# Kernel optimization log

Measured on AMD Instinct MI355X. Metric: run time of the kernel, lower is better.

The kernel has to match this reference:

```python
import jax, jax.numpy as jnp
import numpy as np

N, E, C, H, L, G, K, NC = 50000, 500000, 256, 128, 4, 64, 8, 2
EPS_MSG = 1e-7  # GENConv message eps
EPS_BN = 1e-5   # BatchNorm eps


def setup_inputs() -> dict:
    key = jax.random.key(0)
    ks = jax.random.split(key, 32)
    def nrm(k, shape, scale):
        return jax.random.normal(k, shape, dtype=jnp.float32) * scale
    sC = 1.0 / np.sqrt(C).astype(np.float32)
    sH = 1.0 / np.sqrt(H).astype(np.float32)
    s2H = 1.0 / np.sqrt(2 * H).astype(np.float32)
    return dict(
        x=nrm(ks[0], (N, C), 1.0),
        edge_index=jax.random.randint(ks[1], (2, E), 0, N, dtype=jnp.int32),
        edge_attr=jax.random.uniform(ks[2], (E, 1), dtype=jnp.float32),
        batch=jnp.sort(jax.random.randint(ks[3], (N,), 0, G, dtype=jnp.int32)),
        clinical=nrm(ks[4], (G, K), 1.0),
        lin_src_w=nrm(ks[5], (C, H), sC), lin_src_b=nrm(ks[6], (H,), 0.01),
        lin_dst_w=nrm(ks[7], (C, H), sC), lin_dst_b=nrm(ks[8], (H,), 0.01),
        edge_w=nrm(ks[9], (L, 1, H), 1.0), edge_b=nrm(ks[10], (L, H), 0.01),
        t=0.1 + 0.01 * jax.random.normal(ks[11], (L,), dtype=jnp.float32),
        mlp_w1=nrm(ks[12], (L, H, 2 * H), sH), mlp_b1=nrm(ks[13], (L, 2 * H), 0.01),
        mlp_bn_g=1.0 + nrm(ks[14], (L, 2 * H), 0.1), mlp_bn_b=nrm(ks[15], (L, 2 * H), 0.1),
        mlp_bn_m=nrm(ks[16], (L, 2 * H), 0.1),
        mlp_bn_v=1.0 + jax.random.uniform(ks[17], (L, 2 * H), dtype=jnp.float32),
        mlp_w2=nrm(ks[18], (L, 2 * H, H), s2H), mlp_b2=nrm(ks[19], (L, H), 0.01),
        norm_g=1.0 + nrm(ks[20], (L, H), 0.1), norm_b=nrm(ks[21], (L, H), 0.1),
        norm_m=nrm(ks[22], (L, H), 0.1),
        norm_v=1.0 + jax.random.uniform(ks[23], (L, H), dtype=jnp.float32),
        cls_w=nrm(ks[24], (H + K, NC), 1.0 / np.sqrt(H + K).astype(np.float32)),
        cls_b=nrm(ks[25], (NC,), 0.01),
    )


def _bn(h, g, b, m, v):
    # eval-mode BatchNorm with running stats
    return g * (h - m) * jax.lax.rsqrt(v + EPS_BN) + b


def reference(x, edge_index, edge_attr, batch, clinical,
              lin_src_w, lin_src_b, lin_dst_w, lin_dst_b,
              edge_w, edge_b, t,
              mlp_w1, mlp_b1, mlp_bn_g, mlp_bn_b, mlp_bn_m, mlp_bn_v,
              mlp_w2, mlp_b2, norm_g, norm_b, norm_m, norm_v,
              cls_w, cls_b):
    n = x.shape[0]
    g_count = clinical.shape[0]
    src, dst = edge_index[0], edge_index[1]
    n_layers = t.shape[0]

    def genconv(xs, xd, l):
        # xs: source features feeding messages [N,H]; xd: dst skip features [N,H]
        e = edge_attr @ edge_w[l] + edge_b[l]               # [E,H]
        msg = jax.nn.relu(xs[src] + e) + EPS_MSG            # [E,H]
        z = msg * t[l]
        zmax = jax.ops.segment_max(z, dst, num_segments=n)  # [N,H]
        zmax = jnp.where(jnp.isfinite(zmax), zmax, 0.0)
        ez = jnp.exp(z - zmax[dst])
        denom = jax.ops.segment_sum(ez, dst, num_segments=n)
        agg = jax.ops.segment_sum(msg * ez, dst, num_segments=n) / jnp.maximum(denom, 1e-16)
        out = agg + xd
        # internal MLP [H, 2H, H]: Linear -> BN -> ReLU -> Linear
        hmid = jax.nn.relu(_bn(out @ mlp_w1[l] + mlp_b1[l],
                               mlp_bn_g[l], mlp_bn_b[l], mlp_bn_m[l], mlp_bn_v[l]))
        return hmid @ mlp_w2[l] + mlp_b2[l]

    # layer 0: conv only (per DeepGCN.forward); lin_src / lin_dst project C -> H
    xs0 = x @ lin_src_w + lin_src_b
    xd0 = x @ lin_dst_w + lin_dst_b
    h = genconv(xs0, xd0, 0)

    # layers 1..L-1: res+ block (norm -> act -> conv, residual add); dropout = identity (eval)
    for l in range(1, n_layers):
        r = jax.nn.relu(_bn(h, norm_g[l], norm_b[l], norm_m[l], norm_v[l]))
        h = h + genconv(r, r, l)

    # final norm/act from layer 0
    h = jax.nn.relu(_bn(h, norm_g[0], norm_b[0], norm_m[0], norm_v[0]))

    # global mean pool over graphs
    cnt = jax.ops.segment_sum(jnp.ones((n,), h.dtype), batch, num_segments=g_count)
    pooled = jax.ops.segment_sum(h, batch, num_segments=g_count) / jnp.maximum(cnt, 1.0)[:, None]

    z = jnp.concatenate([pooled, clinical], axis=1)
    return z @ cls_w + cls_b  # [G, num_classes]; squeeze is a no-op for G>1, NC=2
```

## Files before the change

kernel.cpp:

```cpp
#include <hip/hip_runtime.h>
#include <math.h>

#define Nn 50000
#define MPAD 50048
#define Ee 500000
#define Cc 256
#define Hh 128
#define Ll 4
#define Gg 64
#define Kk 8
#define NCc 2

#define NB 196

typedef __attribute__((ext_vector_type(8))) short short8;
typedef __attribute__((ext_vector_type(4))) float f32x4;
typedef __attribute__((ext_vector_type(2))) float f32x2;

__device__ __forceinline__ unsigned short f2bf(float f) {
    union { float f; unsigned int u; } v;
    v.f = f;
    unsigned int u = v.u;
    return (unsigned short)((u + 0x7FFFu + ((u >> 16) & 1u)) >> 16);
}
__device__ __forceinline__ float bf2f(unsigned short s) {
    union { float f; unsigned int u; } v;
    v.u = ((unsigned int)s) << 16;
    return v.f;
}
__device__ __forceinline__ float bf2f_lo(unsigned int u) {
    union { float f; unsigned int u; } v;
    v.u = u << 16;
    return v.f;
}
__device__ __forceinline__ float bf2f_hi(unsigned int u) {
    union { float f; unsigned int u; } v;
    v.u = u & 0xffff0000u;
    return v.f;
}


__global__ void hist_kernel(const int* __restrict__ dst, int* __restrict__ deg) {
    int e = blockIdx.x * 256 + threadIdx.x;
    if (e < Ee) atomicAdd(&deg[dst[e]], 1);
}

__global__ __launch_bounds__(256) void bsum_kernel(const int* __restrict__ deg,
                                                   int* __restrict__ bsum) {
    __shared__ int ws[4];
    int t = threadIdx.x;
    int i = blockIdx.x * 256 + t;
    int v = (i < Nn) ? deg[i] : 0;
#pragma unroll
    for (int o = 32; o; o >>= 1) v += __shfl_down(v, o, 64);
    if ((t & 63) == 0) ws[t >> 6] = v;
    __syncthreads();
    if (t == 0) bsum[blockIdx.x] = ws[0] + ws[1] + ws[2] + ws[3];
}

__global__ __launch_bounds__(256) void bscan_kernel(const int* __restrict__ bsum,
                                                    int* __restrict__ boff,
                                                    int* __restrict__ off) {
    __shared__ int sc[256];
    int t = threadIdx.x;
    int v = (t < NB) ? bsum[t] : 0;
    sc[t] = v;
    __syncthreads();
    for (int o = 1; o < 256; o <<= 1) {
        int u = (t >= o) ? sc[t - o] : 0;
        __syncthreads();
        sc[t] += u;
        __syncthreads();
    }
    if (t < NB) boff[t] = sc[t] - v;
    if (t == NB - 1) off[Nn] = sc[t];
}

__global__ __launch_bounds__(256) void offsets_kernel(const int* __restrict__ deg,
                                                      const int* __restrict__ boff,
                                                      int* __restrict__ off,
                                                      int* __restrict__ pos) {
    __shared__ int sc[256];
    int t = threadIdx.x;
    int i = blockIdx.x * 256 + t;
    int v = (i < Nn) ? deg[i] : 0;
    sc[t] = v;
    __syncthreads();
    for (int o = 1; o < 256; o <<= 1) {
        int u = (t >= o) ? sc[t - o] : 0;
        __syncthreads();
        sc[t] += u;
        __syncthreads();
    }
    int excl = sc[t] - v + boff[blockIdx.x];
    if (i < Nn) {
        off[i] = excl;
        pos[i] = excl;
    }
}

__global__ void scatter_kernel(const int* __restrict__ src, const int* __restrict__ dst,
                               const float* __restrict__ attr, int* __restrict__ pos,
                               int2* __restrict__ sedge) {
    int e = blockIdx.x * 256 + threadIdx.x;
    if (e < Ee) {
        int d = dst[e];
        int p = atomicAdd(&pos[d], 1);
        sedge[p] = make_int2(src[e], __float_as_int(attr[e]));
    }
}


__global__ void wconv_kernel(const float* __restrict__ lin_src_w,
                             const float* __restrict__ lin_dst_w,
                             const float* __restrict__ mlp_w1,
                             const float* __restrict__ mlp_w2,
                             unsigned short* __restrict__ wt) {
    int idx = blockIdx.x * 256 + threadIdx.x;
    if (idx >= 327680) return;
    float val;
    if (idx < 65536) {
        int n = idx >> 8, k = idx & 255;
        val = (n < 128) ? lin_src_w[k * 128 + n] : lin_dst_w[k * 128 + (n - 128)];
    } else if (idx < 196608) {
        int r = idx - 65536;
        int l = r >> 15, e = r & 32767;
        int n = e >> 7, k = e & 127;
        val = mlp_w1[(size_t)l * 32768 + k * 256 + n];
    } else {
        int r = idx - 196608;
        int l = r >> 15, e = r & 32767;
        int n = e >> 8, k = e & 255;
        val = mlp_w2[(size_t)l * 32768 + k * 128 + n];
    }
    wt[idx] = f2bf(val);
}


__global__ __launch_bounds__(256) void xconv_kernel(const float* __restrict__ x,
                                                    unsigned short* __restrict__ xbf) {
    int idx = blockIdx.x * 256 + threadIdx.x;
    if (idx >= (Nn * Cc) / 8) return;
    const float4* p = (const float4*)(x) + (size_t)idx * 2;
    float4 v0 = p[0], v1 = p[1];
    unsigned short t[8];
    t[0] = f2bf(v0.x); t[1] = f2bf(v0.y); t[2] = f2bf(v0.z); t[3] = f2bf(v0.w);
    t[4] = f2bf(v1.x); t[5] = f2bf(v1.y); t[6] = f2bf(v1.z); t[7] = f2bf(v1.w);
    *(short8*)(xbf + (size_t)idx * 8) = *(short8*)t;
}

#define GLOAD16(gp, lp)                                                                       \
    __builtin_amdgcn_global_load_lds(                                                         \
        (const __attribute__((address_space(1))) unsigned int*)(gp),                          \
        (__attribute__((address_space(3))) unsigned int*)(lp), 16, 0, 0)


__global__ __launch_bounds__(256) void proj_kernel(
    const unsigned short* __restrict__ A, const unsigned short* __restrict__ Bt,
    const float* __restrict__ bias, const float* __restrict__ bias2,
    unsigned short* __restrict__ Cout) {
    __shared__ __align__(16) unsigned short SH[24576];
    int tid = threadIdx.x;
    int wave = tid >> 6, lane = tid & 63;
    int wr = wave >> 1, wc = wave & 1;
    int lrow = lane & 15, quad = lane >> 4;
    int m0 = blockIdx.y * 128, n0 = blockIdx.x * 128;
    const int K = 256;

    const unsigned short* ag0 = A + (size_t)(m0 + (tid >> 2)) * K + (tid & 3) * 8;
    const unsigned short* ag1 = A + (size_t)(m0 + 64 + (tid >> 2)) * K + (tid & 3) * 8;
    const unsigned short* bg0 = Bt + (size_t)(n0 + (tid >> 2)) * K + (tid & 3) * 8;
    const unsigned short* bg1 = Bt + (size_t)(n0 + 64 + (tid >> 2)) * K + (tid & 3) * 8;

    f32x4 acc[4][4];
#pragma unroll
    for (int i = 0; i < 4; i++)
#pragma unroll
        for (int j = 0; j < 4; j++) acc[i][j] = (f32x4){0.f, 0.f, 0.f, 0.f};

    auto stage = [&](int buf, int koff) {
        GLOAD16(ag0 + koff, SH + buf * 4096 + wave * 512);
        GLOAD16(ag1 + koff, SH + buf * 4096 + 2048 + wave * 512);
        GLOAD16(bg0 + koff, SH + 12288 + buf * 4096 + wave * 512);
        GLOAD16(bg1 + koff, SH + 12288 + buf * 4096 + 2048 + wave * 512);
    };

    const int ntiles = 8;
    stage(0, 0);
    stage(1, 32);
    for (int t = 0; t < ntiles; ++t) {
        if (t + 1 < ntiles) {
            asm volatile("s_waitcnt vmcnt(4)\n\ts_barrier" ::: "memory");
        } else {
            asm volatile("s_waitcnt vmcnt(0)\n\ts_barrier" ::: "memory");
        }
        if (t + 2 < ntiles) stage((t + 2) % 3, (t + 2) * 32);
        int cur = t % 3;
        const unsigned short* As = SH + cur * 4096;
        const unsigned short* Bs = SH + 12288 + cur * 4096;
        short8 af[4], bfr[4];
#pragma unroll
        for (int mt = 0; mt < 4; mt++)
            af[mt] = *(const short8*)&As[(wr * 64 + mt * 16 + lrow) * 32 + quad * 8];
#pragma unroll
        for (int nf = 0; nf < 4; nf++)
            bfr[nf] = *(const short8*)&Bs[(wc * 64 + nf * 16 + lrow) * 32 + quad * 8];
#pragma unroll
        for (int mt = 0; mt < 4; mt++)
#pragma unroll
            for (int nf = 0; nf < 4; nf++)
                acc[mt][nf] = __builtin_amdgcn_mfma_f32_16x16x32_bf16(af[mt], bfr[nf],
                                                                     acc[mt][nf], 0, 0, 0);
    }

    __syncthreads();
    unsigned short* Cl = SH;
#pragma unroll
    for (int nf = 0; nf < 4; nf++) {
        int gc = n0 + wc * 64 + nf * 16 + lrow;
        float bs = (gc >= 128) ? bias2[gc - 128] : bias[gc];
        int col = wc * 64 + nf * 16 + lrow;
#pragma unroll
        for (int mt = 0; mt < 4; mt++)
#pragma unroll
            for (int r = 0; r < 4; r++)
                Cl[(wr * 64 + mt * 16 + quad * 4 + r) * 128 + col] = f2bf(acc[mt][nf][r] + bs);
    }
    __syncthreads();
#pragma unroll
    for (int p = 0; p < 8; p++) {
        int vid = p * 256 + tid;
        int row = vid >> 4, cg = (vid & 15) * 8;
        short8 v = *(const short8*)&Cl[row * 128 + cg];
        *(short8*)(Cout + (size_t)(m0 + row) * 256 + n0 + cg) = v;
    }
}


__global__ __launch_bounds__(256) void mlp_kernel(
    const unsigned short* __restrict__ A,
    const unsigned short* __restrict__ W1,
    const unsigned short* __restrict__ W2,
    const float* __restrict__ b1, const float* __restrict__ bn_g,
    const float* __restrict__ bn_b, const float* __restrict__ bn_m,
    const float* __restrict__ bn_v, const float* __restrict__ b2,
    const float* __restrict__ pn_g, const float* __restrict__ pn_b,
    const float* __restrict__ pn_m, const float* __restrict__ pn_v,
    float* __restrict__ hbuf, unsigned short* __restrict__ rbuf, int rmw) {
    __shared__ __align__(16) unsigned short S[20480];
    __shared__ __align__(16) unsigned short Hm[64 * 264];

    int tid = threadIdx.x;
    int wave = tid >> 6, lane = tid & 63;
    int lrow = lane & 15, quad = lane >> 4;
    int m0 = blockIdx.x * 64;

    const unsigned short* ag = A + (size_t)(m0 + (tid >> 2)) * 128 + (tid & 3) * 8;
    const unsigned short* bg = W1 + (size_t)(tid >> 2) * 128 + (tid & 3) * 8;

    f32x4 acc1[4][4];
#pragma unroll
    for (int i = 0; i < 4; i++)
#pragma unroll
        for (int j = 0; j < 4; j++) acc1[i][j] = (f32x4){0.f, 0.f, 0.f, 0.f};

    auto stage1 = [&](int buf, int k0) {
        GLOAD16(ag + k0, S + buf * 2048 + wave * 512);
#pragma unroll
        for (int c = 0; c < 4; c++)
            GLOAD16(bg + (size_t)c * 64 * 128 + k0,
                    S + 4096 + buf * 8192 + c * 2048 + wave * 512);
    };

    stage1(0, 0);
    __syncthreads();
    for (int t = 0; t < 4; ++t) {
        if (t + 1 < 4) stage1((t + 1) & 1, (t + 1) * 32);
        int cur = t & 1;
        const unsigned short* A1s = S + cur * 2048;
        const unsigned short* B1s = S + 4096 + cur * 8192;
        short8 af[4], bfr[4];
#pragma unroll
        for (int mt = 0; mt < 4; mt++)
            af[mt] = *(const short8*)&A1s[(mt * 16 + lrow) * 32 + quad * 8];
#pragma unroll
        for (int nf = 0; nf < 4; nf++)
            bfr[nf] = *(const short8*)&B1s[(wave * 64 + nf * 16 + lrow) * 32 + quad * 8];
#pragma unroll
        for (int mt = 0; mt < 4; mt++)
#pragma unroll
            for (int nf = 0; nf < 4; nf++)
                acc1[mt][nf] = __builtin_amdgcn_mfma_f32_16x16x32_bf16(af[mt], bfr[nf],
                                                                      acc1[mt][nf], 0, 0, 0);
        __syncthreads();
    }

#pragma unroll
    for (int nf = 0; nf < 4; nf++) {
        int gc = wave * 64 + nf * 16 + lrow;
        float bs = b1[gc];
        float g = bn_g[gc], bb = bn_b[gc], mm = bn_m[gc];
        float inv = rsqrtf(bn_v[gc] + 1e-5f);
#pragma unroll
        for (int mt = 0; mt < 4; mt++)
#pragma unroll
            for (int r = 0; r < 4; r++) {
                float v = acc1[mt][nf][r] + bs;
                v = fmaxf(g * (v - mm) * inv + bb, 0.f);
                Hm[(mt * 16 + quad * 4 + r) * 264 + gc] = f2bf(v);
            }
    }
    __syncthreads();

    const unsigned short* b2g0 = W2 + (size_t)(tid >> 2) * 256 + (tid & 3) * 8;
    const unsigned short* b2g1 = W2 + (size_t)(64 + (tid >> 2)) * 256 + (tid & 3) * 8;

    f32x4 acc2[4][2];
#pragma unroll
    for (int i = 0; i < 4; i++)
#pragma unroll
        for (int j = 0; j < 2; j++) acc2[i][j] = (f32x4){0.f, 0.f, 0.f, 0.f};

    auto stage2 = [&](int buf, int k0) {
        GLOAD16(b2g0 + k0, S + buf * 4096 + wave * 512);
        GLOAD16(b2g1 + k0, S + buf * 4096 + 2048 + wave * 512);
    };

    stage2(0, 0);
    __syncthreads();
    for (int t = 0; t < 8; ++t) {
        if (t + 1 < 8) stage2((t + 1) & 1, (t + 1) * 32);
        int cur = t & 1;
        const unsigned short* B2s = S + cur * 4096;
        short8 af[4], bfr[2];
#pragma unroll
        for (int mt = 0; mt < 4; mt++)
            af[mt] = *(const short8*)&Hm[(mt * 16 + lrow) * 264 + t * 32 + quad * 8];
#pragma unroll
        for (int nf = 0; nf < 2; nf++)
            bfr[nf] = *(const short8*)&B2s[(wave * 32 + nf * 16 + lrow) * 32 + quad * 8];
#pragma unroll
        for (int mt = 0; mt < 4; mt++)
#pragma unroll
            for (int nf = 0; nf < 2; nf++)
                acc2[mt][nf] = __builtin_amdgcn_mfma_f32_16x16x32_bf16(af[mt], bfr[nf],
                                                                      acc2[mt][nf], 0, 0, 0);
        __syncthreads();
    }

    float* C2 = (float*)S;
#pragma unroll
    for (int nf = 0; nf < 2; nf++) {
        int gc = wave * 32 + nf * 16 + lrow;
        float bs = b2[gc];
#pragma unroll
        for (int mt = 0; mt < 4; mt++)
#pragma unroll
            for (int r = 0; r < 4; r++)
                C2[(mt * 16 + quad * 4 + r) * 128 + gc] = acc2[mt][nf][r] + bs;
    }
    __syncthreads();
#pragma unroll
    for (int p = 0; p < 8; p++) {
        int vid = p * 256 + tid;
        int row = vid >> 5, c4 = (vid & 31) * 4;
        f32x4 v = *(const f32x4*)&C2[row * 128 + c4];
        float* hp = hbuf + (size_t)(m0 + row) * 128 + c4;
        if (rmw) v += *(const f32x4*)hp;
        *(f32x4*)hp = v;
        if (pn_g) {
            f32x4 pg = *(const f32x4*)&pn_g[c4];
            f32x4 pb = *(const f32x4*)&pn_b[c4];
            f32x4 pm = *(const f32x4*)&pn_m[c4];
            f32x4 pv = *(const f32x4*)&pn_v[c4];
            unsigned int w0, w1;
            float r0 = fmaxf(pg[0] * (v[0] - pm[0]) * rsqrtf(pv[0] + 1e-5f) + pb[0], 0.f);
            float r1 = fmaxf(pg[1] * (v[1] - pm[1]) * rsqrtf(pv[1] + 1e-5f) + pb[1], 0.f);
            float r2 = fmaxf(pg[2] * (v[2] - pm[2]) * rsqrtf(pv[2] + 1e-5f) + pb[2], 0.f);
            float r3 = fmaxf(pg[3] * (v[3] - pm[3]) * rsqrtf(pv[3] + 1e-5f) + pb[3], 0.f);
            w0 = (unsigned int)f2bf(r0) | ((unsigned int)f2bf(r1) << 16);
            w1 = (unsigned int)f2bf(r2) | ((unsigned int)f2bf(r3) << 16);
            uint2 pk = make_uint2(w0, w1);
            *(uint2*)(rbuf + (size_t)(m0 + row) * 128 + c4) = pk;
        }
    }
}


template <int XSS>
__global__ __launch_bounds__(256) void agg_kernel(
    const unsigned short* __restrict__ xs,
    const unsigned short* __restrict__ xd, int xds,
    const int2* __restrict__ sedge, const int* __restrict__ off,
    const float* __restrict__ ew, const float* __restrict__ eb,
    const float* __restrict__ tptr, unsigned short* __restrict__ outb) {
    int wave = threadIdx.x >> 6;
    int lane = threadIdx.x & 63;
    int d = blockIdx.x * 4 + wave;
    int s0 = off[d], s1 = off[d + 1];
    int f0 = lane * 2;
    f32x2 wv = *(const f32x2*)(ew + f0);
    f32x2 bv = *(const f32x2*)(eb + f0);
    float c = tptr[0] * 1.44269504088896f;
    const f32x2 zz = {0.f, 0.f};
    const f32x2 ee = {1e-7f, 1e-7f};
    f32x2 den = {0.f, 0.f}, num = {0.f, 0.f};

#define EDGE2(u, av)                                                      \
    {                                                                     \
        f32x2 xv = {bf2f_lo(u), bf2f_hi(u)};                              \
        f32x2 m = __builtin_elementwise_max(xv + bv + (av)*wv, zz) + ee;  \
        f32x2 e;                                                          \
        e.x = __builtin_amdgcn_exp2f(m.x * c);                            \
        e.y = __builtin_amdgcn_exp2f(m.y * c);                            \
        den += e;                                                         \
        num += m * e;                                                     \
    }

    int j = s0;
    for (; j + 3 < s1; j += 4) {
        int2 p0 = sedge[j], p1 = sedge[j + 1], p2 = sedge[j + 2], p3 = sedge[j + 3];
        unsigned int u0 = *(const unsigned int*)(xs + (size_t)p0.x * XSS + f0);
        unsigned int u1 = *(const unsigned int*)(xs + (size_t)p1.x * XSS + f0);
        unsigned int u2 = *(const unsigned int*)(xs + (size_t)p2.x * XSS + f0);
        unsigned int u3 = *(const unsigned int*)(xs + (size_t)p3.x * XSS + f0);
        EDGE2(u0, __int_as_float(p0.y))
        EDGE2(u1, __int_as_float(p1.y))
        EDGE2(u2, __int_as_float(p2.y))
        EDGE2(u3, __int_as_float(p3.y))
    }
    for (; j < s1; j++) {
        int2 p = sedge[j];
        unsigned int u = *(const unsigned int*)(xs + (size_t)p.x * XSS + f0);
        EDGE2(u, __int_as_float(p.y))
    }
#undef EDGE2
    float a0 = (s1 > s0) ? (num.x / fmaxf(den.x, 1e-16f)) : 0.f;
    float a1 = (s1 > s0) ? (num.y / fmaxf(den.y, 1e-16f)) : 0.f;
    unsigned int ud = *(const unsigned int*)(xd + (size_t)d * xds + f0);
    unsigned int lo = f2bf(a0 + bf2f_lo(ud));
    unsigned int hi = f2bf(a1 + bf2f_hi(ud));
    *(unsigned int*)(outb + (size_t)d * Hh + f0) = lo | (hi << 16);
}


#define PCHUNK 100

__global__ __launch_bounds__(128) void pool_kernel(
    const float* __restrict__ h, const int* __restrict__ batch,
    const float* __restrict__ g, const float* __restrict__ b,
    const float* __restrict__ m, const float* __restrict__ v,
    float* __restrict__ pooled, float* __restrict__ cnt) {
    int hh = threadIdx.x;
    int i0 = blockIdx.x * PCHUNK;
    int i1 = min(i0 + PCHUNK, Nn);
    if (i0 >= Nn) return;
    float gg = g[hh], bb = b[hh], mm = m[hh], inv = rsqrtf(v[hh] + 1e-5f);
    int cur = batch[i0];
    float sum = 0.f, c = 0.f;
    for (int i = i0; i < i1; i++) {
        int gid = batch[i];
        float val = fmaxf(gg * (h[(size_t)i * Hh + hh] - mm) * inv + bb, 0.f);
        if (gid != cur) {
            atomicAdd(&pooled[(size_t)cur * Hh + hh], sum);
            if (hh == 0) atomicAdd(&cnt[cur], c);
            cur = gid;
            sum = 0.f;
            c = 0.f;
        }
        sum += val;
        c += 1.f;
    }
    atomicAdd(&pooled[(size_t)cur * Hh + hh], sum);
    if (hh == 0) atomicAdd(&cnt[cur], c);
}


__global__ __launch_bounds__(128) void cls_kernel(const float* __restrict__ pooled,
                                                  const float* __restrict__ cnt,
                                                  const float* __restrict__ clinical,
                                                  const float* __restrict__ w,
                                                  const float* __restrict__ bias,
                                                  float* __restrict__ out) {
    int t = threadIdx.x;
    int g = t >> 1, c = t & 1;
    float inv = 1.f / fmaxf(cnt[g], 1.f);
    float s = bias[c];
    for (int j = 0; j < Hh; j++) s += pooled[g * Hh + j] * inv * w[j * NCc + c];
    for (int k = 0; k < Kk; k++) s += clinical[g * Kk + k] * w[(Hh + k) * NCc + c];
    out[g * NCc + c] = s;
}


extern "C" void kernel_launch(void* const* d_in, const int* in_sizes, int n_in,
                              void* d_out, int out_size, void* d_ws, size_t ws_size,
                              hipStream_t stream) {
    const float* x = (const float*)d_in[0];
    const int* eidx = (const int*)d_in[1];
    const float* eattr = (const float*)d_in[2];
    const int* batch = (const int*)d_in[3];
    const float* clinical = (const float*)d_in[4];
    const float* lin_src_w = (const float*)d_in[5];
    const float* lin_src_b = (const float*)d_in[6];
    const float* lin_dst_w = (const float*)d_in[7];
    const float* lin_dst_b = (const float*)d_in[8];
    const float* edge_w = (const float*)d_in[9];
    const float* edge_b = (const float*)d_in[10];
    const float* tt = (const float*)d_in[11];
    const float* mlp_w1 = (const float*)d_in[12];
    const float* mlp_b1 = (const float*)d_in[13];
    const float* bn_g = (const float*)d_in[14];
    const float* bn_b = (const float*)d_in[15];
    const float* bn_m = (const float*)d_in[16];
    const float* bn_v = (const float*)d_in[17];
    const float* mlp_w2 = (const float*)d_in[18];
    const float* mlp_b2 = (const float*)d_in[19];
    const float* norm_g = (const float*)d_in[20];
    const float* norm_b = (const float*)d_in[21];
    const float* norm_m = (const float*)d_in[22];
    const float* norm_v = (const float*)d_in[23];
    const float* cls_w = (const float*)d_in[24];
    const float* cls_b = (const float*)d_in[25];
    float* out = (float*)d_out;

    const int* src = eidx;
    const int* dst = eidx + Ee;

    char* ws = (char*)d_ws;
    size_t off_b = 0;
    auto alloc = [&](size_t bytes) -> void* {
        void* p = ws + off_b;
        off_b += (bytes + 255) & ~(size_t)255;
        return p;
    };
    unsigned short* xsd = (unsigned short*)alloc((size_t)MPAD * 256 * 2);
    unsigned short* rbuf = (unsigned short*)alloc((size_t)MPAD * Hh * 2);
    unsigned short* aggout = (unsigned short*)alloc((size_t)MPAD * Hh * 2);
    unsigned short* xbf = (unsigned short*)alloc((size_t)MPAD * 256 * 2);
    float* hbuf = (float*)alloc((size_t)MPAD * Hh * 4);
    int* deg = (int*)alloc((Nn + 1) * 4);
    int* offp = (int*)alloc((Nn + 1) * 4);
    int* pos = (int*)alloc((size_t)Nn * 4);
    int* bsum = (int*)alloc(NB * 4);
    int* boff = (int*)alloc(NB * 4);
    int2* sedge = (int2*)alloc((size_t)Ee * 8);
    float* pooled = (float*)alloc((size_t)Gg * Hh * 4);
    float* cntb = (float*)alloc(Gg * 4);
    unsigned short* wt = (unsigned short*)alloc((size_t)327680 * 2);

    hipMemsetAsync(deg, 0, (Nn + 1) * 4, stream);
    hipMemsetAsync(pooled, 0, (size_t)Gg * Hh * 4, stream);
    hipMemsetAsync(cntb, 0, Gg * 4, stream);

    hist_kernel<<<(Ee + 255) / 256, 256, 0, stream>>>(dst, deg);
    bsum_kernel<<<NB, 256, 0, stream>>>(deg, bsum);
    bscan_kernel<<<1, 256, 0, stream>>>(bsum, boff, offp);
    offsets_kernel<<<NB, 256, 0, stream>>>(deg, boff, offp, pos);
    scatter_kernel<<<(Ee + 255) / 256, 256, 0, stream>>>(src, dst, eattr, pos, sedge);
    wconv_kernel<<<1280, 256, 0, stream>>>(lin_src_w, lin_dst_w, mlp_w1, mlp_w2, wt);
    xconv_kernel<<<(Nn * Cc / 8 + 255) / 256, 256, 0, stream>>>(x, xbf);

    const unsigned short* wt_proj = wt;
    const unsigned short* wt_w1 = wt + 65536;
    const unsigned short* wt_w2 = wt + 196608;

    dim3 gproj(2, MPAD / 128);
    proj_kernel<<<gproj, 256, 0, stream>>>(xbf, wt_proj, lin_src_b, lin_dst_b, xsd);

    for (int l = 0; l < Ll; l++) {
        if (l == 0) {
            agg_kernel<256><<<Nn / 4, 256, 0, stream>>>(xsd, xsd + 128, 256, sedge, offp,
                                                        edge_w + l * Hh, edge_b + l * Hh,
                                                        tt + l, aggout);
        } else {
            agg_kernel<128><<<Nn / 4, 256, 0, stream>>>(rbuf, rbuf, Hh, sedge, offp,
                                                        edge_w + l * Hh, edge_b + l * Hh,
                                                        tt + l, aggout);
        }
        const float* png = (l < Ll - 1) ? (norm_g + (l + 1) * Hh) : nullptr;
        const float* pnb = (l < Ll - 1) ? (norm_b + (l + 1) * Hh) : nullptr;
        const float* pnm = (l < Ll - 1) ? (norm_m + (l + 1) * Hh) : nullptr;
        const float* pnv = (l < Ll - 1) ? (norm_v + (l + 1) * Hh) : nullptr;
        mlp_kernel<<<MPAD / 64, 256, 0, stream>>>(
            aggout, wt_w1 + (size_t)l * 32768, wt_w2 + (size_t)l * 32768,
            mlp_b1 + l * 2 * Hh, bn_g + l * 2 * Hh, bn_b + l * 2 * Hh,
            bn_m + l * 2 * Hh, bn_v + l * 2 * Hh, mlp_b2 + l * Hh,
            png, pnb, pnm, pnv, hbuf, rbuf, (l == 0) ? 0 : 1);
    }

    pool_kernel<<<(Nn + PCHUNK - 1) / PCHUNK, 128, 0, stream>>>(hbuf, batch, norm_g, norm_b,
                                                                norm_m, norm_v, pooled, cntb);
    cls_kernel<<<1, 128, 0, stream>>>(pooled, cntb, clinical, cls_w, cls_b, out);
}
```

Measured before the change: 509.8 us.

## Fuse edge aggregation into per-layer MLP kernel with ping-pong activation buffers

Merges the softmax edge-aggregation kernel and the MLP kernel into one layer kernel. Each 64-row block first aggregates its destination nodes into LDS, then runs both GEMMs from LDS, so the aggregated tile no longer makes a round trip through global memory and one launch per layer is removed. Weight fragments are now read straight from global memory instead of being staged in LDS with double buffering. The relu(bn) output alternates between two buffers because other blocks still read the previous layer's activations. Risks: only 782 blocks of 256 threads, each wave aggregating 16 nodes serially, which gives less latency hiding for the gathers than the old one-node-per-wave launch.

```diff
diff --git a/kernel.cpp b/kernel.cpp
--- a/kernel.cpp
+++ b/kernel.cpp
@@ -237,8 +237,17 @@
 }
 
 
-__global__ __launch_bounds__(256) void mlp_kernel(
-    const unsigned short* __restrict__ A,
+#define AGP 136
+#define HMP 264
+#define C2P 132
+
+template <int XSS>
+__global__ __launch_bounds__(256) void layer_kernel(
+    const unsigned short* __restrict__ xs,
+    const unsigned short* __restrict__ xd, int xds,
+    const int2* __restrict__ sedge, const int* __restrict__ off,
+    const float* __restrict__ ew, const float* __restrict__ eb,
+    const float* __restrict__ tptr,
     const unsigned short* __restrict__ W1,
     const unsigned short* __restrict__ W2,
     const float* __restrict__ b1, const float* __restrict__ bn_g,
@@ -246,55 +255,90 @@
     const float* __restrict__ bn_v, const float* __restrict__ b2,
     const float* __restrict__ pn_g, const float* __restrict__ pn_b,
     const float* __restrict__ pn_m, const float* __restrict__ pn_v,
-    float* __restrict__ hbuf, unsigned short* __restrict__ rbuf, int rmw) {
-    __shared__ __align__(16) unsigned short S[20480];
-    __shared__ __align__(16) unsigned short Hm[64 * 264];
+    float* __restrict__ hbuf, unsigned short* __restrict__ rout, int rmw) {
+    __shared__ __align__(16) unsigned short Agg[64 * AGP];
+    __shared__ __align__(16) unsigned short Hm[64 * HMP];
 
     int tid = threadIdx.x;
     int wave = tid >> 6, lane = tid & 63;
     int lrow = lane & 15, quad = lane >> 4;
     int m0 = blockIdx.x * 64;
 
-    const unsigned short* ag = A + (size_t)(m0 + (tid >> 2)) * 128 + (tid & 3) * 8;
-    const unsigned short* bg = W1 + (size_t)(tid >> 2) * 128 + (tid & 3) * 8;
+    {
+        int f0 = lane * 2;
+        f32x2 wv = *(const f32x2*)(ew + f0);
+        f32x2 bv = *(const f32x2*)(eb + f0);
+        float cc = tptr[0] * 1.44269504088896f;
+        const f32x2 zz = {0.f, 0.f};
+        const f32x2 ee = {1e-7f, 1e-7f};
+#define EDGE2(u, av)                                                      \
+    {                                                                     \
+        f32x2 xv = {bf2f_lo(u), bf2f_hi(u)};                              \
+        f32x2 m = __builtin_elementwise_max(xv + bv + (av)*wv, zz) + ee;  \
+        f32x2 e;                                                          \
+        e.x = __builtin_amdgcn_exp2f(m.x * cc);                           \
+        e.y = __builtin_amdgcn_exp2f(m.y * cc);                           \
+        den += e;                                                         \
+        num += m * e;                                                     \
+    }
+        for (int nn = 0; nn < 16; nn++) {
+            int d = m0 + wave * 16 + nn;
+            int s0 = 0, s1 = 0;
+            if (d < Nn) {
+                s0 = off[d];
+                s1 = off[d + 1];
+            }
+            f32x2 den = {0.f, 0.f}, num = {0.f, 0.f};
+            int j = s0;
+            for (; j + 3 < s1; j += 4) {
+                int2 p0 = sedge[j], p1 = sedge[j + 1], p2 = sedge[j + 2], p3 = sedge[j + 3];
+                unsigned int u0 = *(const unsigned int*)(xs + (size_t)p0.x * XSS + f0);
+                unsigned int u1 = *(const unsigned int*)(xs + (size_t)p1.x * XSS + f0);
+                unsigned int u2 = *(const unsigned int*)(xs + (size_t)p2.x * XSS + f0);
+                unsigned int u3 = *(const unsigned int*)(xs + (size_t)p3.x * XSS + f0);
+                EDGE2(u0, __int_as_float(p0.y))
+                EDGE2(u1, __int_as_float(p1.y))
+                EDGE2(u2, __int_as_float(p2.y))
+                EDGE2(u3, __int_as_float(p3.y))
+            }
+            for (; j < s1; j++) {
+                int2 p = sedge[j];
+                unsigned int u = *(const unsigned int*)(xs + (size_t)p.x * XSS + f0);
+                EDGE2(u, __int_as_float(p.y))
+            }
+            float a0 = (s1 > s0) ? (num.x / fmaxf(den.x, 1e-16f)) : 0.f;
+            float a1 = (s1 > s0) ? (num.y / fmaxf(den.y, 1e-16f)) : 0.f;
+            unsigned int ud = *(const unsigned int*)(xd + (size_t)d * xds + f0);
+            unsigned int lo = f2bf(a0 + bf2f_lo(ud));
+            unsigned int hi = f2bf(a1 + bf2f_hi(ud));
+            *(unsigned int*)&Agg[(wave * 16 + nn) * AGP + f0] = lo | (hi << 16);
+        }
+#undef EDGE2
+    }
+    __syncthreads();
 
     f32x4 acc1[4][4];
 #pragma unroll
     for (int i = 0; i < 4; i++)
 #pragma unroll
         for (int j = 0; j < 4; j++) acc1[i][j] = (f32x4){0.f, 0.f, 0.f, 0.f};
-
-    auto stage1 = [&](int buf, int k0) {
-        GLOAD16(ag + k0, S + buf * 2048 + wave * 512);
-#pragma unroll
-        for (int c = 0; c < 4; c++)
-            GLOAD16(bg + (size_t)c * 64 * 128 + k0,
-                    S + 4096 + buf * 8192 + c * 2048 + wave * 512);
-    };
-
-    stage1(0, 0);
-    __syncthreads();
-    for (int t = 0; t < 4; ++t) {
-        if (t + 1 < 4) stage1((t + 1) & 1, (t + 1) * 32);
-        int cur = t & 1;
-        const unsigned short* A1s = S + cur * 2048;
-        const unsigned short* B1s = S + 4096 + cur * 8192;
+#pragma unroll
+    for (int t = 0; t < 4; t++) {
         short8 af[4], bfr[4];
 #pragma unroll
         for (int mt = 0; mt < 4; mt++)
-            af[mt] = *(const short8*)&A1s[(mt * 16 + lrow) * 32 + quad * 8];
+            af[mt] = *(const short8*)&Agg[(mt * 16 + lrow) * AGP + t * 32 + quad * 8];
 #pragma unroll
         for (int nf = 0; nf < 4; nf++)
-            bfr[nf] = *(const short8*)&B1s[(wave * 64 + nf * 16 + lrow) * 32 + quad * 8];
+            bfr[nf] = *(const short8*)(W1 + (size_t)(wave * 64 + nf * 16 + lrow) * 128 +
+                                       t * 32 + quad * 8);
 #pragma unroll
         for (int mt = 0; mt < 4; mt++)
 #pragma unroll
             for (int nf = 0; nf < 4; nf++)
                 acc1[mt][nf] = __builtin_amdgcn_mfma_f32_16x16x32_bf16(af[mt], bfr[nf],
                                                                       acc1[mt][nf], 0, 0, 0);
-        __syncthreads();
-    }
-
+    }
 #pragma unroll
     for (int nf = 0; nf < 4; nf++) {
         int gc = wave * 64 + nf * 16 + lrow;
@@ -307,48 +351,36 @@
             for (int r = 0; r < 4; r++) {
                 float v = acc1[mt][nf][r] + bs;
                 v = fmaxf(g * (v - mm) * inv + bb, 0.f);
-                Hm[(mt * 16 + quad * 4 + r) * 264 + gc] = f2bf(v);
+                Hm[(mt * 16 + quad * 4 + r) * HMP + gc] = f2bf(v);
             }
     }
     __syncthreads();
 
-    const unsigned short* b2g0 = W2 + (size_t)(tid >> 2) * 256 + (tid & 3) * 8;
-    const unsigned short* b2g1 = W2 + (size_t)(64 + (tid >> 2)) * 256 + (tid & 3) * 8;
-
     f32x4 acc2[4][2];
 #pragma unroll
     for (int i = 0; i < 4; i++)
 #pragma unroll
         for (int j = 0; j < 2; j++) acc2[i][j] = (f32x4){0.f, 0.f, 0.f, 0.f};
-
-    auto stage2 = [&](int buf, int k0) {
-        GLOAD16(b2g0 + k0, S + buf * 4096 + wave * 512);
-        GLOAD16(b2g1 + k0, S + buf * 4096 + 2048 + wave * 512);
-    };
-
-    stage2(0, 0);
-    __syncthreads();
-    for (int t = 0; t < 8; ++t) {
-        if (t + 1 < 8) stage2((t + 1) & 1, (t + 1) * 32);
-        int cur = t & 1;
-        const unsigned short* B2s = S + cur * 4096;
+#pragma unroll
+    for (int t = 0; t < 8; t++) {
         short8 af[4], bfr[2];
 #pragma unroll
         for (int mt = 0; mt < 4; mt++)
-            af[mt] = *(const short8*)&Hm[(mt * 16 + lrow) * 264 + t * 32 + quad * 8];
+            af[mt] = *(const short8*)&Hm[(mt * 16 + lrow) * HMP + t * 32 + quad * 8];
 #pragma unroll
         for (int nf = 0; nf < 2; nf++)
-            bfr[nf] = *(const short8*)&B2s[(wave * 32 + nf * 16 + lrow) * 32 + quad * 8];
+            bfr[nf] = *(const short8*)(W2 + (size_t)(wave * 32 + nf * 16 + lrow) * 256 +
+                                       t * 32 + quad * 8);
 #pragma unroll
         for (int mt = 0; mt < 4; mt++)
 #pragma unroll
             for (int nf = 0; nf < 2; nf++)
                 acc2[mt][nf] = __builtin_amdgcn_mfma_f32_16x16x32_bf16(af[mt], bfr[nf],
                                                                       acc2[mt][nf], 0, 0, 0);
-        __syncthreads();
-    }
-
-    float* C2 = (float*)S;
+    }
+    __syncthreads();
+
+    float* C2 = (float*)Hm;
 #pragma unroll
     for (int nf = 0; nf < 2; nf++) {
         int gc = wave * 32 + nf * 16 + lrow;
@@ -357,14 +389,14 @@
         for (int mt = 0; mt < 4; mt++)
 #pragma unroll
             for (int r = 0; r < 4; r++)
-                C2[(mt * 16 + quad * 4 + r) * 128 + gc] = acc2[mt][nf][r] + bs;
+                C2[(mt * 16 + quad * 4 + r) * C2P + gc] = acc2[mt][nf][r] + bs;
     }
     __syncthreads();
 #pragma unroll
     for (int p = 0; p < 8; p++) {
         int vid = p * 256 + tid;
         int row = vid >> 5, c4 = (vid & 31) * 4;
-        f32x4 v = *(const f32x4*)&C2[row * 128 + c4];
+        f32x4 v = *(const f32x4*)&C2[row * C2P + c4];
         float* hp = hbuf + (size_t)(m0 + row) * 128 + c4;
         if (rmw) v += *(const f32x4*)hp;
         *(f32x4*)hp = v;
@@ -373,74 +405,16 @@
             f32x4 pb = *(const f32x4*)&pn_b[c4];
             f32x4 pm = *(const f32x4*)&pn_m[c4];
             f32x4 pv = *(const f32x4*)&pn_v[c4];
-            unsigned int w0, w1;
             float r0 = fmaxf(pg[0] * (v[0] - pm[0]) * rsqrtf(pv[0] + 1e-5f) + pb[0], 0.f);
             float r1 = fmaxf(pg[1] * (v[1] - pm[1]) * rsqrtf(pv[1] + 1e-5f) + pb[1], 0.f);
             float r2 = fmaxf(pg[2] * (v[2] - pm[2]) * rsqrtf(pv[2] + 1e-5f) + pb[2], 0.f);
             float r3 = fmaxf(pg[3] * (v[3] - pm[3]) * rsqrtf(pv[3] + 1e-5f) + pb[3], 0.f);
-            w0 = (unsigned int)f2bf(r0) | ((unsigned int)f2bf(r1) << 16);
-            w1 = (unsigned int)f2bf(r2) | ((unsigned int)f2bf(r3) << 16);
+            unsigned int w0 = (unsigned int)f2bf(r0) | ((unsigned int)f2bf(r1) << 16);
+            unsigned int w1 = (unsigned int)f2bf(r2) | ((unsigned int)f2bf(r3) << 16);
             uint2 pk = make_uint2(w0, w1);
-            *(uint2*)(rbuf + (size_t)(m0 + row) * 128 + c4) = pk;
+            *(uint2*)(rout + (size_t)(m0 + row) * 128 + c4) = pk;
         }
     }
-}
-
-
-template <int XSS>
-__global__ __launch_bounds__(256) void agg_kernel(
-    const unsigned short* __restrict__ xs,
-    const unsigned short* __restrict__ xd, int xds,
-    const int2* __restrict__ sedge, const int* __restrict__ off,
-    const float* __restrict__ ew, const float* __restrict__ eb,
-    const float* __restrict__ tptr, unsigned short* __restrict__ outb) {
-    int wave = threadIdx.x >> 6;
-    int lane = threadIdx.x & 63;
-    int d = blockIdx.x * 4 + wave;
-    int s0 = off[d], s1 = off[d + 1];
-    int f0 = lane * 2;
-    f32x2 wv = *(const f32x2*)(ew + f0);
-    f32x2 bv = *(const f32x2*)(eb + f0);
-    float c = tptr[0] * 1.44269504088896f;
-    const f32x2 zz = {0.f, 0.f};
-    const f32x2 ee = {1e-7f, 1e-7f};
-    f32x2 den = {0.f, 0.f}, num = {0.f, 0.f};
-
-#define EDGE2(u, av)                                                      \
-    {                                                                     \
-        f32x2 xv = {bf2f_lo(u), bf2f_hi(u)};                              \
-        f32x2 m = __builtin_elementwise_max(xv + bv + (av)*wv, zz) + ee;  \
-        f32x2 e;                                                          \
-        e.x = __builtin_amdgcn_exp2f(m.x * c);                            \
-        e.y = __builtin_amdgcn_exp2f(m.y * c);                            \
-        den += e;                                                         \
-        num += m * e;                                                     \
-    }
-
-    int j = s0;
-    for (; j + 3 < s1; j += 4) {
-        int2 p0 = sedge[j], p1 = sedge[j + 1], p2 = sedge[j + 2], p3 = sedge[j + 3];
-        unsigned int u0 = *(const unsigned int*)(xs + (size_t)p0.x * XSS + f0);
-        unsigned int u1 = *(const unsigned int*)(xs + (size_t)p1.x * XSS + f0);
-        unsigned int u2 = *(const unsigned int*)(xs + (size_t)p2.x * XSS + f0);
-        unsigned int u3 = *(const unsigned int*)(xs + (size_t)p3.x * XSS + f0);
-        EDGE2(u0, __int_as_float(p0.y))
-        EDGE2(u1, __int_as_float(p1.y))
-        EDGE2(u2, __int_as_float(p2.y))
-        EDGE2(u3, __int_as_float(p3.y))
-    }
-    for (; j < s1; j++) {
-        int2 p = sedge[j];
-        unsigned int u = *(const unsigned int*)(xs + (size_t)p.x * XSS + f0);
-        EDGE2(u, __int_as_float(p.y))
-    }
-#undef EDGE2
-    float a0 = (s1 > s0) ? (num.x / fmaxf(den.x, 1e-16f)) : 0.f;
-    float a1 = (s1 > s0) ? (num.y / fmaxf(den.y, 1e-16f)) : 0.f;
-    unsigned int ud = *(const unsigned int*)(xd + (size_t)d * xds + f0);
-    unsigned int lo = f2bf(a0 + bf2f_lo(ud));
-    unsigned int hi = f2bf(a1 + bf2f_hi(ud));
-    *(unsigned int*)(outb + (size_t)d * Hh + f0) = lo | (hi << 16);
 }
 
 
@@ -534,8 +508,8 @@
         return p;
     };
     unsigned short* xsd = (unsigned short*)alloc((size_t)MPAD * 256 * 2);
-    unsigned short* rbuf = (unsigned short*)alloc((size_t)MPAD * Hh * 2);
-    unsigned short* aggout = (unsigned short*)alloc((size_t)MPAD * Hh * 2);
+    unsigned short* rb0 = (unsigned short*)alloc((size_t)MPAD * Hh * 2);
+    unsigned short* rb1 = (unsigned short*)alloc((size_t)MPAD * Hh * 2);
     unsigned short* xbf = (unsigned short*)alloc((size_t)MPAD * 256 * 2);
     float* hbuf = (float*)alloc((size_t)MPAD * Hh * 4);
     int* deg = (int*)alloc((Nn + 1) * 4);
@@ -567,25 +541,27 @@
     dim3 gproj(2, MPAD / 128);
     proj_kernel<<<gproj, 256, 0, stream>>>(xbf, wt_proj, lin_src_b, lin_dst_b, xsd);
 
+    unsigned short* rb[2] = {rb0, rb1};
     for (int l = 0; l < Ll; l++) {
-        if (l == 0) {
-            agg_kernel<256><<<Nn / 4, 256, 0, stream>>>(xsd, xsd + 128, 256, sedge, offp,
-                                                        edge_w + l * Hh, edge_b + l * Hh,
-                                                        tt + l, aggout);
-        } else {
-            agg_kernel<128><<<Nn / 4, 256, 0, stream>>>(rbuf, rbuf, Hh, sedge, offp,
-                                                        edge_w + l * Hh, edge_b + l * Hh,
-                                                        tt + l, aggout);
-        }
         const float* png = (l < Ll - 1) ? (norm_g + (l + 1) * Hh) : nullptr;
         const float* pnb = (l < Ll - 1) ? (norm_b + (l + 1) * Hh) : nullptr;
         const float* pnm = (l < Ll - 1) ? (norm_m + (l + 1) * Hh) : nullptr;
         const float* pnv = (l < Ll - 1) ? (norm_v + (l + 1) * Hh) : nullptr;
-        mlp_kernel<<<MPAD / 64, 256, 0, stream>>>(
-            aggout, wt_w1 + (size_t)l * 32768, wt_w2 + (size_t)l * 32768,
-            mlp_b1 + l * 2 * Hh, bn_g + l * 2 * Hh, bn_b + l * 2 * Hh,
-            bn_m + l * 2 * Hh, bn_v + l * 2 * Hh, mlp_b2 + l * Hh,
-            png, pnb, pnm, pnv, hbuf, rbuf, (l == 0) ? 0 : 1);
+        unsigned short* rout = rb[l & 1];
+        const unsigned short* rin = rb[1 - (l & 1)];
+        if (l == 0) {
+            layer_kernel<256><<<MPAD / 64, 256, 0, stream>>>(
+                xsd, xsd + 128, 256, sedge, offp, edge_w, edge_b, tt,
+                wt_w1, wt_w2, mlp_b1, bn_g, bn_b, bn_m, bn_v, mlp_b2,
+                png, pnb, pnm, pnv, hbuf, rout, 0);
+        } else {
+            layer_kernel<128><<<MPAD / 64, 256, 0, stream>>>(
+                rin, rin, 128, sedge, offp, edge_w + l * Hh, edge_b + l * Hh, tt + l,
+                wt_w1 + (size_t)l * 32768, wt_w2 + (size_t)l * 32768,
+                mlp_b1 + l * 2 * Hh, bn_g + l * 2 * Hh, bn_b + l * 2 * Hh,
+                bn_m + l * 2 * Hh, bn_v + l * 2 * Hh, mlp_b2 + l * Hh,
+                png, pnb, pnm, pnv, hbuf, rout, 1);
+        }
     }
 
     pool_kernel<<<(Nn + PCHUNK - 1) / PCHUNK, 128, 0, stream>>>(hbuf, batch, norm_g, norm_b,
```

New measurement: 754.1 us. 1.48x slower.
